# Optimization experiments

Measured on AMD Instinct MI355X. Metric: run time of the kernel, lower is better.

## Reference

```python
import jax, jax.numpy as jnp
import numpy as np

B, N, T, F, K = 32, 24, 12, 3, 3
COUT = 12                      # must equal T (LayerNorm applied to last dim = T)
DIN = N * COUT + N + 1         # 313 = lstm_in_dim
H = DIN * T                    # 3756 = lstm_hidden_dim (forced by residual add)
ODIM = 1
LN_EPS = 1e-5


def setup_inputs() -> dict:
    key = jax.random.key(0)
    ks = jax.random.split(key, 24)
    r = lambda i, shape, s=0.1: jax.random.normal(ks[i], shape, dtype=jnp.float32) * s
    return {
        "X": r(0, (B, N, T, F), 1.0),
        "cheb": r(1, (K, N, N), 0.3),
        # Spatial_Attention_layer (ASTGCN-style) params
        "sa_W1": r(2, (T,)), "sa_W2": r(3, (F, T)), "sa_W3": r(4, (F,)),
        "sa_bs": r(5, (1, N, N)), "sa_Vs": r(6, (N, N)),
        # Temporal_Attention_layer params
        "ta_U1": r(7, (N,)), "ta_U2": r(8, (F, N)), "ta_U3": r(9, (F,)),
        "ta_be": r(10, (1, T, T)), "ta_Ve": r(11, (T, T)),
        # ChebConv_with_sa params
        "theta": r(12, (K, F, COUT)), "cheb_bias": jnp.zeros((COUT,), jnp.float32),
        # LayerNorm
        "ln_g": jnp.ones((COUT,), jnp.float32), "ln_b": jnp.zeros((COUT,), jnp.float32),
        # layer_in: Linear(seq_len, seq_len)
        "layer_in_w": r(13, (T, T)), "layer_in_b": r(14, (T,)),
        # S_A2: Linear(lstm_in_dim, lstm_in_dim)
        "sa2_w": r(15, (DIN, DIN), 0.05), "sa2_b": r(16, (DIN,)),
        # LSTMCell (torch gate order i,f,g,o)
        "W_ih": r(17, (4 * H, DIN), 0.02), "W_hh": r(18, (4 * H, H), 0.01),
        "b_ih": jnp.zeros((4 * H,), jnp.float32), "b_hh": jnp.zeros((4 * H,), jnp.float32),
        # T_A2: Linear(seq_len*hidden, seq_len)
        "ta2_w": r(19, (T, T * H), 0.02), "ta2_b": r(20, (T,)),
        # layer_out
        "out_w": r(21, (ODIM, H), 0.02), "out_b": jnp.zeros((ODIM,), jnp.float32),
        # torch.randn initial states (fixed here for determinism)
        "h0": r(22, (B, H), 1.0), "c0": r(23, (B, H), 1.0),
    }


def reference(X, cheb, sa_W1, sa_W2, sa_W3, sa_bs, sa_Vs,
              ta_U1, ta_U2, ta_U3, ta_be, ta_Ve,
              theta, cheb_bias, ln_g, ln_b,
              layer_in_w, layer_in_b, sa2_w, sa2_b,
              W_ih, W_hh, b_ih, b_hh, ta2_w, ta2_b,
              out_w, out_b, h0, c0):
    sig = jax.nn.sigmoid
    Bsz = X.shape[0]
    x_flow = X[:, 0:1, :, 1]                     # (B,1,T)
    x_rain = X[:, :, :, 0]                       # (B,N,T)
    x_pre = jnp.concatenate([x_rain, x_flow], axis=1)  # (B,N+1,T)
    x4 = jnp.transpose(X, (0, 1, 3, 2))          # (B,N,F,T)

    # spatial attention; legacy nn.Softmax() on 3D tensor => axis=0
    lhs = jnp.einsum('bnf,ft->bnt', jnp.einsum('bnft,t->bnf', x4, sa_W1), sa_W2)
    rhs = jnp.einsum('f,bnft->btn', sa_W3, x4)
    S = jnp.einsum('nm,bmk->bnk', sa_Vs, sig(jnp.einsum('bnt,btm->bnm', lhs, rhs) + sa_bs))
    s_a = jax.nn.softmax(sig(jax.nn.softmax(S, axis=1)), axis=0)   # (B,N,N)

    # temporal attention
    xp = jnp.transpose(x4, (0, 3, 2, 1))         # (B,T,F,N)
    lhs_t = jnp.einsum('btf,fn->btn', jnp.einsum('btfn,n->btf', xp, ta_U1), ta_U2)
    rhs_t = jnp.einsum('f,bnft->bnt', ta_U3, x4)
    E = jnp.einsum('tu,buv->btv', ta_Ve, sig(jnp.einsum('btn,bnu->btu', lhs_t, rhs_t) + ta_be))
    t_a = jax.nn.softmax(sig(jax.nn.softmax(E, axis=1)), axis=0)   # (B,T,T)

    # attention-weighted Chebyshev conv; note reshape (not transpose), as in original
    xg = X.reshape(Bsz, N, F, -1)                # (B,N,F,T)
    Tk_at = cheb[None] * s_a[:, None]            # (B,K,N,N)
    rhs_g = jnp.einsum('bkmn,bmft->bknft', Tk_at, xg)
    xc = jax.nn.relu(jnp.einsum('bknft,kfo->bnot', rhs_g, theta) + cheb_bias[:, None])  # (B,N,COUT,T)

    # LayerNorm over last dim (T == COUT)
    mu = xc.mean(-1, keepdims=True)
    var = xc.var(-1, keepdims=True)
    x_ln = (xc - mu) / jnp.sqrt(var + LN_EPS) * ln_g + ln_b

    x_gc = x_ln.reshape(Bsz, -1, 12)             # (B, N*COUT, 12)
    x_gc_t = jnp.einsum('bij,bjk->bik', x_gc, t_a)
    x_res = jnp.concatenate([x_gc_t, x_pre], axis=1)   # (B, DIN, 12)
    x_in = x_res @ layer_in_w.T + layer_in_b     # Linear over last (seq) dim
    xs = jnp.transpose(x_in, (2, 0, 1))          # (T, B, DIN)

    def step(carry, x_t):
        h, c = carry
        alpha = jax.nn.softmax(sig(x_t @ sa2_w.T + sa2_b), axis=1)
        xi = x_t * alpha + x_t
        gates = xi @ W_ih.T + b_ih + h @ W_hh.T + b_hh
        i, f, g, o = jnp.split(gates, 4, axis=1)
        c2 = sig(f) * c + sig(i) * jnp.tanh(g)
        h2 = sig(o) * jnp.tanh(c2)
        return (h2, c2), h2

    _, hs = jax.lax.scan(step, (h0, c0), xs)     # (T,B,H)
    total_ht = jnp.transpose(hs, (1, 0, 2)).reshape(Bsz, -1)  # cat along dim 1, time-major
    beta = jax.nn.softmax(jax.nn.relu(total_ht @ ta2_w.T + ta2_b), axis=1)  # (B,T)
    out = jnp.einsum('tbh,bt->bh', hs, beta)
    out = out + x_in.reshape(Bsz, -1)            # requires H == DIN*T
    out = jax.nn.relu(out) @ out_w.T + out_b
    return out, s_a
```

## Files before the change

kernel.cpp:

```cpp
#include <hip/hip_runtime.h>

#define BSZ 32
#define NN 24
#define TT 12
#define FF 3
#define KK 3
#define COUT 12
#define DIN 313
#define HID 3756
#define H4 15024
#define KP 3776
#define KPI 320
#define NTILES 470
#define NB 235
#define NCH 30

using short8 = __attribute__((ext_vector_type(8))) short;
using f32x4  = __attribute__((ext_vector_type(4))) float;

__device__ inline unsigned short f2bf(float f){
  union{float f; unsigned u;} v; v.f=f;
  unsigned u=v.u;
  return (unsigned short)((u + 0x7FFFu + ((u>>16)&1u))>>16);
}
__device__ inline f32x4 mfma16(short8 a, short8 b, f32x4 c){
  return __builtin_amdgcn_mfma_f32_16x16x32_bf16(a,b,c,0,0,0);
}
__device__ inline float sigm(float x){ return 1.f/(1.f+expf(-x)); }

__device__ void conv_slab(const float* __restrict__ W, unsigned short* __restrict__ Wp,
    int bi, int cg0, int cg1, int tid, int nthr, unsigned short* lds){
  for(int cg=cg0; cg<cg1; cg++){
    int ks0=cg*4;
    int nks=min(4,118-ks0);
    int nf4=nks*8;
    for(int q=tid;q<64*nf4;q+=nthr){
      int r=q/nf4, f4=q-r*nf4;
      int g=r>>4, lj=r&15;
      int jj=bi*16+lj; if(jj>=HID) jj=HID-1;
      const float* src=W+(long)(g*HID+jj)*HID;
      int k=ks0*32+f4*4;
      ushort4 o;
      if(k+3<HID){
        float4 v=*(const float4*)(src+k);
        o.x=f2bf(v.x); o.y=f2bf(v.y); o.z=f2bf(v.z); o.w=f2bf(v.w);
      } else {
        float vv[4];
        #pragma unroll
        for(int t2=0;t2<4;t2++){ int kk=k+t2; vv[t2]=(kk<HID)?src[kk]:0.f; }
        o.x=f2bf(vv[0]); o.y=f2bf(vv[1]); o.z=f2bf(vv[2]); o.w=f2bf(vv[3]);
      }
      *(ushort4*)(&lds[r*136+f4*4])=o;
    }
    __syncthreads();
    for(int idx=tid; idx<nks*4*64; idx+=nthr){
      int l=idx&63, g=(idx>>6)&3, kl=idx>>8;
      int lj=l&15, lk=l>>4;
      short8 v=*(short8*)(&lds[(g*16+lj)*136 + kl*32 + lk*8]);
      *(short8*)(Wp + (((long)(bi*118+ks0+kl)*4+g)*64 + l)*8) = v;
    }
    __syncthreads();
  }
}

__global__ void __launch_bounds__(256) k_f1(const float* __restrict__ X,
   const float* __restrict__ sa_W1, const float* __restrict__ sa_W2,
   const float* __restrict__ sa_W3, const float* __restrict__ sa_bs,
   const float* __restrict__ sa_Vs, const float* __restrict__ ta_U1,
   const float* __restrict__ ta_U2, const float* __restrict__ ta_U3,
   const float* __restrict__ ta_be, const float* __restrict__ ta_Ve,
   float* __restrict__ SA_pre, float* __restrict__ TA_pre,
   const float* __restrict__ W, unsigned short* __restrict__ Wp){
  __shared__ __align__(16) float smf[4352];
  int tid=threadIdx.x;
  if(blockIdx.x>=32){
    conv_slab(W,Wp,blockIdx.x-32,0,8,tid,256,(unsigned short*)smf);
    return;
  }
  int b=blockIdx.x;
  float* lin=smf;        float* lhs=smf+864;   float* rhs=smf+1152;
  float* P=smf+1440;     float* S=smf+2016;    float* lhsT=smf+2592;
  float* rhsT=smf+2880;  float* PT=smf+3168;   float* E=smf+3312;
  for(int i=tid;i<864;i+=256) lin[i]=X[b*864+i];
  __syncthreads();
  for(int i=tid;i<NN*TT;i+=256){ int n=i/TT, t=i%TT;
    float acc=0;
    #pragma unroll
    for(int f=0;f<FF;f++){
      float t1=0;
      for(int u=0;u<TT;u++) t1 += lin[n*36+u*3+f]*sa_W1[u];
      acc += t1*sa_W2[f*TT+t];
    }
    lhs[n*TT+t]=acc;
    float r=0;
    #pragma unroll
    for(int f=0;f<FF;f++) r += sa_W3[f]*lin[n*36+t*3+f];
    rhs[t*NN+n]=r;
  }
  for(int i=tid;i<TT*NN;i+=256){ int t=i/NN, n=i%NN;
    float acc=0;
    #pragma unroll
    for(int f=0;f<FF;f++){
      float t1=0;
      for(int m=0;m<NN;m++) t1 += lin[m*36+t*3+f]*ta_U1[m];
      acc += t1*ta_U2[f*NN+n];
    }
    lhsT[t*NN+n]=acc;
    float r=0;
    #pragma unroll
    for(int f=0;f<FF;f++) r += ta_U3[f]*lin[n*36+t*3+f];
    rhsT[n*TT+t]=r;
  }
  __syncthreads();
  for(int i=tid;i<NN*NN;i+=256){ int n=i/NN,m=i%NN;
    float a=0;
    for(int t=0;t<TT;t++) a+=lhs[n*TT+t]*rhs[t*NN+m];
    P[i]=sigm(a+sa_bs[i]);
  }
  for(int i=tid;i<TT*TT;i+=256){ int t=i/TT,u=i%TT;
    float a=0;
    for(int n=0;n<NN;n++) a+=lhsT[t*NN+n]*rhsT[n*TT+u];
    PT[i]=sigm(a+ta_be[i]);
  }
  __syncthreads();
  for(int i=tid;i<NN*NN;i+=256){ int n=i/NN,k=i%NN;
    float a=0;
    for(int m=0;m<NN;m++) a+=sa_Vs[n*NN+m]*P[m*NN+k];
    S[i]=a;
  }
  for(int i=tid;i<TT*TT;i+=256){ int t=i/TT,v=i%TT;
    float a=0;
    for(int u=0;u<TT;u++) a+=ta_Ve[t*TT+u]*PT[u*TT+v];
    E[i]=a;
  }
  __syncthreads();
  if(tid<NN){ int k=tid;
    float mx=-1e30f;
    for(int n=0;n<NN;n++) mx=fmaxf(mx,S[n*NN+k]);
    float sm=0;
    for(int n=0;n<NN;n++) sm+=__expf(S[n*NN+k]-mx);
    for(int n=0;n<NN;n++){
      float v=__expf(S[n*NN+k]-mx)/sm;
      SA_pre[b*576+n*NN+k]=sigm(v);
    }
  }
  if(tid>=32 && tid<32+TT){ int v=tid-32;
    float mx=-1e30f;
    for(int t=0;t<TT;t++) mx=fmaxf(mx,E[t*TT+v]);
    float sm=0;
    for(int t=0;t<TT;t++) sm+=__expf(E[t*TT+v]-mx);
    for(int t=0;t<TT;t++){
      float e=__expf(E[t*TT+v]-mx)/sm;
      TA_pre[b*144+t*TT+v]=sigm(e);
    }
  }
}

__global__ void __launch_bounds__(320) k_f2(const float* __restrict__ X,
  const float* __restrict__ cheb, const float* __restrict__ SA_pre,
  const float* __restrict__ TA_pre, const float* __restrict__ theta,
  const float* __restrict__ cheb_bias, const float* __restrict__ ln_g,
  const float* __restrict__ ln_b, const float* __restrict__ liw,
  const float* __restrict__ lib, float* __restrict__ x_in,
  float* __restrict__ out_sa,
  const float* __restrict__ W, unsigned short* __restrict__ Wp){
  __shared__ __align__(16) float smf[13116];
  int tid=threadIdx.x;
  if(blockIdx.x>=32){
    conv_slab(W,Wp,blockIdx.x-32,8,16,tid,320,(unsigned short*)smf);
    return;
  }
  int b=blockIdx.x;
  float* lin =smf;
  float* A2  =smf+864;
  float* rg  =smf+2592;
  float* xc  =smf+5184;
  float* xres=smf+8640;
  float* tal =smf+12396;
  float* sa_l=smf+12540;
  for(int i=tid;i<864;i+=320) lin[i]=X[b*864+i];
  for(int i=tid;i<576;i+=320){
    float mx=-1e30f;
    for(int bb=0;bb<BSZ;bb++) mx=fmaxf(mx,SA_pre[bb*576+i]);
    float sm=0;
    for(int bb=0;bb<BSZ;bb++) sm+=__expf(SA_pre[bb*576+i]-mx);
    float v=__expf(SA_pre[b*576+i]-mx)/sm;
    sa_l[i]=v;
    out_sa[b*576+i]=v;
  }
  for(int i=tid;i<144;i+=320){
    float mx=-1e30f;
    for(int bb=0;bb<BSZ;bb++) mx=fmaxf(mx,TA_pre[bb*144+i]);
    float sm=0;
    for(int bb=0;bb<BSZ;bb++) sm+=__expf(TA_pre[bb*144+i]-mx);
    tal[i]=__expf(TA_pre[b*144+i]-mx)/sm;
  }
  __syncthreads();
  for(int i=tid;i<KK*NN*NN;i+=320){ int mn=i%576; A2[i]=cheb[i]*sa_l[mn]; }
  __syncthreads();
  for(int i=tid;i<KK*NN*FF*TT;i+=320){
    int t=i%TT, f=(i/TT)%FF, n=(i/36)%NN, k=i/864;
    float a=0;
    for(int m=0;m<NN;m++) a+=A2[k*576+m*NN+n]*lin[m*36+f*TT+t];
    rg[i]=a;
  }
  __syncthreads();
  for(int i=tid;i<NN*COUT*TT;i+=320){
    int t=i%TT, o=(i/TT)%COUT, n=i/(COUT*TT);
    float a=cheb_bias[o];
    #pragma unroll
    for(int k=0;k<KK;k++)
      #pragma unroll
      for(int f=0;f<FF;f++)
        a += rg[((k*NN+n)*FF+f)*TT+t]*theta[(k*FF+f)*COUT+o];
    xc[i]=fmaxf(a,0.f);
  }
  __syncthreads();
  if(tid<NN*COUT){
    float mu=0;
    for(int t=0;t<TT;t++) mu+=xc[tid*TT+t];
    mu*=(1.f/12.f);
    float var=0;
    for(int t=0;t<TT;t++){ float d=xc[tid*TT+t]-mu; var+=d*d; }
    var*=(1.f/12.f);
    float inv=rsqrtf(var+1e-5f);
    for(int t=0;t<TT;t++) xc[tid*TT+t]=(xc[tid*TT+t]-mu)*inv*ln_g[t]+ln_b[t];
  }
  __syncthreads();
  for(int i=tid;i<NN*COUT;i+=320){
    for(int v=0;v<TT;v++){
      float a=0;
      for(int t=0;t<TT;t++) a+=xc[i*TT+t]*tal[t*TT+v];
      xres[i*TT+v]=a;
    }
  }
  for(int i=tid;i<25*TT;i+=320){
    int r=i/TT, t=i%TT;
    float v=(r<NN)? lin[r*36+t*3+0] : lin[t*3+1];
    xres[(288+r)*TT+t]=v;
  }
  __syncthreads();
  for(int i=tid;i<DIN;i+=320){
    for(int t=0;t<TT;t++){
      float a=lib[t];
      #pragma unroll
      for(int u=0;u<TT;u++) a+=xres[i*TT+u]*liw[t*TT+u];
      x_in[((long)b*DIN+i)*TT+t]=a;
    }
  }
}

__global__ void __launch_bounds__(512) k_f3(const float* __restrict__ x_in,
    const float* __restrict__ sa2_w, const float* __restrict__ sa2_b,
    unsigned short* __restrict__ xi_b,
    const float* __restrict__ W, unsigned short* __restrict__ Wp){
  __shared__ __align__(16) float smf[4352];
  int tid=threadIdx.x;
  if(blockIdx.x>=384){
    conv_slab(W,Wp,blockIdx.x-384,16,23,tid,512,(unsigned short*)smf);
    return;
  }
  int blk=blockIdx.x; int t=blk>>5, b=blk&31;
  float* xt=smf;
  float* red=smf+320;
  if(tid<DIN) xt[tid]=x_in[((long)b*DIN+tid)*TT+t];
  __syncthreads();
  float z=-1e30f, e=0.f;
  if(tid<DIN){
    float a=sa2_b[tid];
    const float* wr=sa2_w+(long)tid*DIN;
    for(int i=0;i<DIN;i++) a+=xt[i]*wr[i];
    z=sigm(a);
  }
  red[tid]=z; __syncthreads();
  for(int off=256;off>0;off>>=1){ if(tid<off) red[tid]=fmaxf(red[tid],red[tid+off]); __syncthreads(); }
  float mx=red[0]; __syncthreads();
  e=(tid<DIN)?__expf(z-mx):0.f;
  red[tid]=e; __syncthreads();
  for(int off=256;off>0;off>>=1){ if(tid<off) red[tid]+=red[tid+off]; __syncthreads(); }
  float sm=red[0];
  if(tid<KPI){
    unsigned short v=0;
    if(tid<DIN){
      float alpha=e/sm;
      v=f2bf(xt[tid]*alpha+xt[tid]);
    }
    xi_b[(long)blk*KPI+tid]=v;
  }
}

__global__ void __launch_bounds__(256) k_f4(const unsigned short* __restrict__ xi,
   const float* __restrict__ Wih, const float* __restrict__ b_ih,
   const float* __restrict__ b_hh, float* __restrict__ Gx,
   const float* __restrict__ W, unsigned short* __restrict__ Wp,
   const float* __restrict__ h0f, unsigned short* __restrict__ hb0,
   unsigned short* __restrict__ hb1){
  __shared__ __align__(16) float smf[4352];
  int tid=threadIdx.x;
  if(blockIdx.x>=118){
    int cb_=blockIdx.x-118;
    conv_slab(W,Wp,cb_,23,30,tid,256,(unsigned short*)smf);
    const int g4=KP>>2;
    for(int i=cb_*256+tid; i<BSZ*g4; i+=NB*256){
      int gq=i%g4, r=i/g4;
      int k=gq*4;
      float vv[4];
      if(k+3<HID){
        float4 x=*(const float4*)(h0f+(long)r*HID+k);
        vv[0]=x.x; vv[1]=x.y; vv[2]=x.z; vv[3]=x.w;
      } else {
        #pragma unroll
        for(int q=0;q<4;q++){ int kk=k+q; vv[q]=(kk<HID)? h0f[(long)r*HID+kk] : 0.f; }
      }
      ushort4 o;
      o.x=f2bf(vv[0]); o.y=f2bf(vv[1]); o.z=f2bf(vv[2]); o.w=f2bf(vv[3]);
      *(ushort4*)(hb0+(long)r*KP+k)=o;
      *(ushort4*)(hb1+(long)r*KP+k)=o;
    }
    return;
  }
  int w=tid>>6, lane=tid&63;
  int jt=blockIdx.x*4+w;
  if(jt>=NTILES) return;
  int j0=jt*32;
  int lj=lane&15, lk=lane>>4;
  short8 bfr[10][2];
  #pragma unroll
  for(int ks=0;ks<10;ks++)
    #pragma unroll
    for(int jh=0;jh<2;jh++){
      int j=j0+jh*16+lj;
      short8 bv;
      #pragma unroll
      for(int q=0;q<8;q++){
        int k=ks*32+lk*8+q;
        float f=(j<H4 && k<DIN)? Wih[(long)j*DIN+k] : 0.f;
        bv[q]=(short)f2bf(f);
      }
      bfr[ks][jh]=bv;
    }
  for(int t=0;t<TT;t++){
    f32x4 acc[2][2]={};
    #pragma unroll
    for(int ks=0;ks<10;ks++){
      #pragma unroll
      for(int mh=0;mh<2;mh++){
        short8 a=*(const short8*)(xi + ((long)(t*32+mh*16+lj))*KPI + ks*32 + lk*8);
        acc[mh][0]=mfma16(a,bfr[ks][0],acc[mh][0]);
        acc[mh][1]=mfma16(a,bfr[ks][1],acc[mh][1]);
      }
    }
    #pragma unroll
    for(int mh=0;mh<2;mh++)
      #pragma unroll
      for(int jh=0;jh<2;jh++){
        int j=j0+jh*16+lj;
        if(j<H4){
          float bias=b_ih[j]+b_hh[j];
          #pragma unroll
          for(int r=0;r<4;r++){
            int bb=mh*16+lk*4+r;
            Gx[((long)t*32+bb)*H4+j]=acc[mh][jh][r]+bias;
          }
        }
      }
  }
}

__global__ void __launch_bounds__(512) k_step(const unsigned short* __restrict__ hb_r,
    unsigned short* __restrict__ hb_w, const unsigned short* __restrict__ Wp,
    const float* __restrict__ Gx, const float* __restrict__ c0,
    float* __restrict__ c, float* __restrict__ hs, int t){
  const int tid=threadIdx.x;
  const int w=tid>>6, lane=tid&63;
  const int j0=blockIdx.x*16;
  const int lj=lane&15, lk=lane>>4;
  const int s0=(118*w)>>3, s1=(118*(w+1))>>3;
  const unsigned short* slab = Wp + (long)blockIdx.x*64*KP;
  f32x4 acc[4][2]={};
  #pragma unroll 2
  for(int ks=s0;ks<s1;ks++){
    int kofs=ks*32+lk*8;
    short8 a0=*(const short8*)(hb_r + (long)lj*KP + kofs);
    short8 a1=*(const short8*)(hb_r + (long)(16+lj)*KP + kofs);
    const unsigned short* pk = slab + ((long)ks<<11);
    #pragma unroll
    for(int g=0;g<4;g++){
      short8 bv=*(const short8*)(pk + (g<<9) + (lane<<3));
      acc[g][0]=mfma16(a0,bv,acc[g][0]);
      acc[g][1]=mfma16(a1,bv,acc[g][1]);
    }
  }
  __shared__ float red[8][4][512];
  #pragma unroll
  for(int g=0;g<4;g++)
    #pragma unroll
    for(int mh=0;mh<2;mh++)
      #pragma unroll
      for(int r=0;r<4;r++)
        red[w][g][(mh*16+lk*4+r)*16+lj]=acc[g][mh][r];
  __syncthreads();
  if(tid<512){
    int p=tid;
    int bb=p>>4, jl=p&15; int j=j0+jl;
    if(j<HID){
      long gxo=((long)t*BSZ+bb)*H4 + j;
      float si=0,sf=0,sg=0,so=0;
      #pragma unroll
      for(int ww=0;ww<8;ww++){
        si+=red[ww][0][p]; sf+=red[ww][1][p];
        sg+=red[ww][2][p]; so+=red[ww][3][p];
      }
      si+=Gx[gxo]; sf+=Gx[gxo+HID]; sg+=Gx[gxo+2*HID]; so+=Gx[gxo+3*HID];
      float gi=sigm(si), gf=sigm(sf), gg=tanhf(sg), go=sigm(so);
      int idx=bb*HID+j;
      float cin=(t==0)?c0[idx]:c[idx];
      float c2=gf*cin+gi*gg;
      float h2=go*tanhf(c2);
      c[idx]=c2;
      hs[(long)t*BSZ*HID+idx]=h2;
      hb_w[(long)bb*KP+j]=f2bf(h2);
    }
  }
}

__global__ void k_tail(const float* __restrict__ hs, const float* __restrict__ ta2_w,
   const float* __restrict__ ta2_b, const float* __restrict__ x_in,
   const float* __restrict__ out_w, const float* __restrict__ out_b,
   float* __restrict__ out0){
  int b=blockIdx.x, tid=threadIdx.x;
  float p[12]={0,0,0,0,0,0,0,0,0,0,0,0};
  for(int idx=tid; idx<TT*HID; idx+=256){
    int t=idx/HID, j=idx-t*HID;
    float v=hs[((long)t*BSZ+b)*HID+j];
    #pragma unroll
    for(int q=0;q<12;q++) p[q]+=v*ta2_w[(long)q*TT*HID+idx];
  }
  __shared__ float red[256];
  __shared__ float bt[12];
  float z[12];
  #pragma unroll
  for(int q=0;q<12;q++){
    __syncthreads();
    red[tid]=p[q]; __syncthreads();
    for(int off=128;off>0;off>>=1){ if(tid<off) red[tid]+=red[tid+off]; __syncthreads(); }
    z[q]=red[0];
  }
  if(tid==0){
    float mx=-1e30f;
    #pragma unroll
    for(int q=0;q<12;q++){ z[q]=fmaxf(z[q]+ta2_b[q],0.f); mx=fmaxf(mx,z[q]); }
    float sm=0;
    #pragma unroll
    for(int q=0;q<12;q++){ z[q]=__expf(z[q]-mx); sm+=z[q]; }
    #pragma unroll
    for(int q=0;q<12;q++) bt[q]=z[q]/sm;
  }
  __syncthreads();
  float acc=0;
  for(int j=tid;j<HID;j+=256){
    float ov=0;
    #pragma unroll
    for(int t=0;t<TT;t++) ov+=hs[((long)t*BSZ+b)*HID+j]*bt[t];
    ov+=x_in[(long)b*HID+j];
    acc+=fmaxf(ov,0.f)*out_w[j];
  }
  __syncthreads();
  red[tid]=acc; __syncthreads();
  for(int off=128;off>0;off>>=1){ if(tid<off) red[tid]+=red[tid+off]; __syncthreads(); }
  if(tid==0) out0[b]=red[0]+out_b[0];
}

extern "C" void kernel_launch(void* const* d_in, const int* in_sizes, int n_in,
                              void* d_out, int out_size, void* d_ws, size_t ws_size,
                              hipStream_t stream){
  (void)in_sizes; (void)n_in; (void)out_size; (void)ws_size;
  const float* X     =(const float*)d_in[0];
  const float* cheb  =(const float*)d_in[1];
  const float* sa_W1 =(const float*)d_in[2];
  const float* sa_W2 =(const float*)d_in[3];
  const float* sa_W3 =(const float*)d_in[4];
  const float* sa_bs =(const float*)d_in[5];
  const float* sa_Vs =(const float*)d_in[6];
  const float* ta_U1 =(const float*)d_in[7];
  const float* ta_U2 =(const float*)d_in[8];
  const float* ta_U3 =(const float*)d_in[9];
  const float* ta_be =(const float*)d_in[10];
  const float* ta_Ve =(const float*)d_in[11];
  const float* theta =(const float*)d_in[12];
  const float* cb    =(const float*)d_in[13];
  const float* ln_g  =(const float*)d_in[14];
  const float* ln_b  =(const float*)d_in[15];
  const float* liw   =(const float*)d_in[16];
  const float* lib   =(const float*)d_in[17];
  const float* sa2_w =(const float*)d_in[18];
  const float* sa2_b =(const float*)d_in[19];
  const float* W_ih  =(const float*)d_in[20];
  const float* W_hh  =(const float*)d_in[21];
  const float* b_ih  =(const float*)d_in[22];
  const float* b_hh  =(const float*)d_in[23];
  const float* ta2_w =(const float*)d_in[24];
  const float* ta2_b =(const float*)d_in[25];
  const float* out_w =(const float*)d_in[26];
  const float* out_b =(const float*)d_in[27];
  const float* h0    =(const float*)d_in[28];
  const float* c0    =(const float*)d_in[29];

  char* w=(char*)d_ws;
  unsigned short* Wp =(unsigned short*)(w);
  float* Gx   =(float*)(w+113582080);
  float* hs   =(float*)(w+136658944);
  unsigned short* hb0=(unsigned short*)(w+142428160);
  unsigned short* hb1=(unsigned short*)(w+142669824);
  float* c    =(float*)(w+142911488);
  float* x_in =(float*)(w+143392256);
  unsigned short* xi_b=(unsigned short*)(w+143873024);
  float* SA   =(float*)(w+144118784);
  float* TA   =(float*)(w+144192512);
  float* out_f=(float*)d_out;

  k_f1<<<32+NB,256,0,stream>>>(X,sa_W1,sa_W2,sa_W3,sa_bs,sa_Vs,ta_U1,ta_U2,ta_U3,ta_be,ta_Ve,
                               SA,TA,W_hh,Wp);
  k_f2<<<32+NB,320,0,stream>>>(X,cheb,SA,TA,theta,cb,ln_g,ln_b,liw,lib,x_in,out_f+32,W_hh,Wp);
  k_f3<<<384+NB,512,0,stream>>>(x_in,sa2_w,sa2_b,xi_b,W_hh,Wp);
  k_f4<<<118+NB,256,0,stream>>>(xi_b,W_ih,b_ih,b_hh,Gx,W_hh,Wp,h0,hb0,hb1);
  unsigned short* hb[2]={hb0,hb1};
  for(int t=0;t<TT;t++)
    k_step<<<NB,512,0,stream>>>(hb[t&1],hb[(t+1)&1],Wp,Gx,c0,c,hs,t);
  k_tail<<<32,256,0,stream>>>(hs,ta2_w,ta2_b,x_in,out_w,out_b,out_f);
}
```

Before: 577.8 us.

## Prepack W_ih to bf16 MFMA layout and transpose sa2_w in earlier kernels

```diff
diff --git a/kernel.cpp b/kernel.cpp
--- a/kernel.cpp
+++ b/kernel.cpp
@@ -63,6 +63,33 @@
   }
 }
 
+__device__ void pack_ih(const float* __restrict__ Wih, unsigned short* __restrict__ Wip,
+    int jt, int tid, int nthr, unsigned short* lds ){
+  int j0=jt*32;
+  for(int q=tid;q<32*80;q+=nthr){
+    int r=q/80, f4=q-r*80;
+    int j=j0+r;
+    int k=f4*4;
+    ushort4 o;
+    if(j<H4){
+      const float* src=Wih+(long)j*DIN;
+      float vv[4];
+      #pragma unroll
+      for(int t2=0;t2<4;t2++){ int kk=k+t2; vv[t2]=(kk<DIN)?src[kk]:0.f; }
+      o.x=f2bf(vv[0]); o.y=f2bf(vv[1]); o.z=f2bf(vv[2]); o.w=f2bf(vv[3]);
+    } else { o.x=0;o.y=0;o.z=0;o.w=0; }
+    *(ushort4*)(&lds[r*328+k])=o;
+  }
+  __syncthreads();
+  for(int u=tid;u<1280;u+=nthr){
+    int l=u&63, jh=(u>>6)&1, ks=u>>7;
+    int lj=l&15, lk=l>>4;
+    short8 v=*(short8*)(&lds[(jh*16+lj)*328 + ks*32 + lk*8]);
+    *(short8*)(Wip + (((long)(jt*10+ks)*2+jh)*512) + l*8)=v;
+  }
+  __syncthreads();
+}
+
 __global__ void __launch_bounds__(256) k_f1(const float* __restrict__ X,
    const float* __restrict__ sa_W1, const float* __restrict__ sa_W2,
    const float* __restrict__ sa_W3, const float* __restrict__ sa_bs,
@@ -70,9 +97,19 @@
    const float* __restrict__ ta_U2, const float* __restrict__ ta_U3,
    const float* __restrict__ ta_be, const float* __restrict__ ta_Ve,
    float* __restrict__ SA_pre, float* __restrict__ TA_pre,
-   const float* __restrict__ W, unsigned short* __restrict__ Wp){
-  __shared__ __align__(16) float smf[4352];
+   const float* __restrict__ W, unsigned short* __restrict__ Wp,
+   const float* __restrict__ Wih, unsigned short* __restrict__ Wip){
+  __shared__ __align__(16) float smf[5248];
   int tid=threadIdx.x;
+  if(blockIdx.x>=267){
+    int cb=blockIdx.x-267;
+    #pragma unroll
+    for(int s=0;s<4;s++){
+      int jt=cb*4+s;
+      if(jt<NTILES) pack_ih(Wih,Wip,jt,tid,256,(unsigned short*)smf);
+    }
+    return;
+  }
   if(blockIdx.x>=32){
     conv_slab(W,Wp,blockIdx.x-32,0,8,tid,256,(unsigned short*)smf);
     return;
@@ -163,9 +200,18 @@
   const float* __restrict__ ln_b, const float* __restrict__ liw,
   const float* __restrict__ lib, float* __restrict__ x_in,
   float* __restrict__ out_sa,
-  const float* __restrict__ W, unsigned short* __restrict__ Wp){
+  const float* __restrict__ W, unsigned short* __restrict__ Wp,
+  const float* __restrict__ sa2_w, float* __restrict__ sa2_wT){
   __shared__ __align__(16) float smf[13116];
   int tid=threadIdx.x;
+  if(blockIdx.x>=267){
+    int cb=blockIdx.x-267;
+    for(int idx=cb*320+tid; idx<DIN*DIN; idx+=40*320){
+      int i=idx/DIN, j=idx-i*DIN;
+      sa2_wT[idx]=sa2_w[(long)j*DIN+i];
+    }
+    return;
+  }
   if(blockIdx.x>=32){
     conv_slab(W,Wp,blockIdx.x-32,8,16,tid,320,(unsigned short*)smf);
     return;
@@ -251,7 +297,7 @@
 }
 
 __global__ void __launch_bounds__(512) k_f3(const float* __restrict__ x_in,
-    const float* __restrict__ sa2_w, const float* __restrict__ sa2_b,
+    const float* __restrict__ sa2_wT, const float* __restrict__ sa2_b,
     unsigned short* __restrict__ xi_b,
     const float* __restrict__ W, unsigned short* __restrict__ Wp){
   __shared__ __align__(16) float smf[4352];
@@ -268,8 +314,7 @@
   float z=-1e30f, e=0.f;
   if(tid<DIN){
     float a=sa2_b[tid];
-    const float* wr=sa2_w+(long)tid*DIN;
-    for(int i=0;i<DIN;i++) a+=xt[i]*wr[i];
+    for(int i=0;i<DIN;i++) a+=xt[i]*sa2_wT[(long)i*DIN+tid];
     z=sigm(a);
   }
   red[tid]=z; __syncthreads();
@@ -290,7 +335,7 @@
 }
 
 __global__ void __launch_bounds__(256) k_f4(const unsigned short* __restrict__ xi,
-   const float* __restrict__ Wih, const float* __restrict__ b_ih,
+   const unsigned short* __restrict__ Wip, const float* __restrict__ b_ih,
    const float* __restrict__ b_hh, float* __restrict__ Gx,
    const float* __restrict__ W, unsigned short* __restrict__ Wp,
    const float* __restrict__ h0f, unsigned short* __restrict__ hb0,
@@ -324,21 +369,13 @@
   if(jt>=NTILES) return;
   int j0=jt*32;
   int lj=lane&15, lk=lane>>4;
+  const unsigned short* wslab = Wip + (long)jt*10240;
   short8 bfr[10][2];
   #pragma unroll
   for(int ks=0;ks<10;ks++)
     #pragma unroll
-    for(int jh=0;jh<2;jh++){
-      int j=j0+jh*16+lj;
-      short8 bv;
-      #pragma unroll
-      for(int q=0;q<8;q++){
-        int k=ks*32+lk*8+q;
-        float f=(j<H4 && k<DIN)? Wih[(long)j*DIN+k] : 0.f;
-        bv[q]=(short)f2bf(f);
-      }
-      bfr[ks][jh]=bv;
-    }
+    for(int jh=0;jh<2;jh++)
+      bfr[ks][jh]=*(const short8*)(wslab + ((ks*2+jh)<<9) + (lane<<3));
   for(int t=0;t<TT;t++){
     f32x4 acc[2][2]={};
     #pragma unroll
@@ -517,13 +554,16 @@
   unsigned short* xi_b=(unsigned short*)(w+143873024);
   float* SA   =(float*)(w+144118784);
   float* TA   =(float*)(w+144192512);
+  unsigned short* Wip=(unsigned short*)(w+144211968);
+  float* sa2T =(float*)(w+153837568);
   float* out_f=(float*)d_out;
 
-  k_f1<<<32+NB,256,0,stream>>>(X,sa_W1,sa_W2,sa_W3,sa_bs,sa_Vs,ta_U1,ta_U2,ta_U3,ta_be,ta_Ve,
-                               SA,TA,W_hh,Wp);
-  k_f2<<<32+NB,320,0,stream>>>(X,cheb,SA,TA,theta,cb,ln_g,ln_b,liw,lib,x_in,out_f+32,W_hh,Wp);
-  k_f3<<<384+NB,512,0,stream>>>(x_in,sa2_w,sa2_b,xi_b,W_hh,Wp);
-  k_f4<<<118+NB,256,0,stream>>>(xi_b,W_ih,b_ih,b_hh,Gx,W_hh,Wp,h0,hb0,hb1);
+  k_f1<<<385,256,0,stream>>>(X,sa_W1,sa_W2,sa_W3,sa_bs,sa_Vs,ta_U1,ta_U2,ta_U3,ta_be,ta_Ve,
+                             SA,TA,W_hh,Wp,W_ih,Wip);
+  k_f2<<<307,320,0,stream>>>(X,cheb,SA,TA,theta,cb,ln_g,ln_b,liw,lib,x_in,out_f+32,W_hh,Wp,
+                             sa2_w,sa2T);
+  k_f3<<<384+NB,512,0,stream>>>(x_in,sa2T,sa2_b,xi_b,W_hh,Wp);
+  k_f4<<<118+NB,256,0,stream>>>(xi_b,Wip,b_ih,b_hh,Gx,W_hh,Wp,h0,hb0,hb1);
   unsigned short* hb[2]={hb0,hb1};
   for(int t=0;t<TT;t++)
     k_step<<<NB,512,0,stream>>>(hb[t&1],hb[(t+1)&1],Wp,Gx,c0,c,hs,t);
```

New measurement: 555.6 us. -3.8%, faster.
